# Performance work log

Hardware: AMD Instinct MI355X
Metric: run time of the kernel (lower is better)

Reference implementation:

```python
import jax, jax.numpy as jnp
import numpy as np

KERNEL_SIZE = 5
GROUP_SIZE = 1
SCALE = 2


def setup_inputs() -> dict:
    key = jax.random.key(0)
    k1, k2 = jax.random.split(key)
    N, C, H, W = 2, 256, 128, 128
    features = jax.random.normal(k1, (N, C, H, W), dtype=jnp.float32)
    masks = jax.random.uniform(
        k2, (N, KERNEL_SIZE * KERNEL_SIZE * GROUP_SIZE, H * SCALE, W * SCALE),
        dtype=jnp.float32)
    return {"features": features, "masks": masks}


def reference(features, masks):
    # CARAFE: content-aware reassembly upsampling.
    # out[n,c,i,j] = sum_{dy,dx} feat[n,c, i//s + dy - r, j//s + dx - r]
    #                * masks[n, g*K*K + dy*K + dx, i, j]
    K, G, s = KERNEL_SIZE, GROUP_SIZE, SCALE
    N, C, H, W = features.shape
    Cg = C // G
    K2 = K * K
    r = K // 2
    # zero-pad spatially and gather all K*K shifted views -> (N, C, K2, H, W)
    fp = jnp.pad(features, ((0, 0), (0, 0), (r, r), (r, r)))
    patches = jnp.stack(
        [fp[:, :, dy:dy + H, dx:dx + W] for dy in range(K) for dx in range(K)],
        axis=2)
    patches = patches.reshape(N, G, Cg, K2, H, W)
    # masks at output resolution; split each output pixel into (src_pixel, subpixel)
    m = masks.reshape(N, G, K2, H, s, W, s)
    # weighted reduce over the kernel window, broadcast over channels in group
    out = jnp.einsum('ngckhw,ngkhawb->ngchawb', patches, m)
    return out.reshape(N, C, H * s, W * s)
```

## Files before the change

### kernel.cpp

```cpp
#include <hip/hip_runtime.h>

#define KK 5
#define RR 2
#define N_ 2
#define C_ 256
#define H_ 128
#define W_ 128
#define H2 256
#define W2 256
#define TH 16
#define TW 16
#define CCHUNK 8
#define PH 20
#define PW 20
#define PHPW 400
#define HW (H_*W_)
#define HW2 (H2*W2)
#define DEPTH 4

__global__ __launch_bounds__(256) void carafe_kernel(
    const float* __restrict__ feat,
    const float* __restrict__ masks,
    float* __restrict__ out)
{
    __shared__ float patch[2 * PHPW * 4];

    const int tid = threadIdx.x;
    const int tx = tid & 15;
    const int ty = tid >> 4;

    const int chunk = blockIdx.x & 31;
    const int tile  = blockIdx.x >> 5;
    const int bx = tile & 7;
    const int by = tile >> 3;
    const int c0 = chunk * CCHUNK;
    const int n  = blockIdx.y;

    const int i0 = by * TH + ty;
    const int j0 = bx * TW + tx;
    const int gy0 = by * TH - RR;
    const int gx0 = bx * TW - RR;

    const float* fbase = feat + (size_t)(n * C_ + c0) * HW;
    #pragma unroll
    for (int r = 0; r < 4; ++r) {
        const int idx = tid + r * 256;
        if (idx < 2 * PHPW) {
            const int G  = idx / PHPW;
            const int p  = idx - G * PHPW;
            const int py = p / PW;
            const int px = p - py * PW;
            const int gy = gy0 + py;
            const int gx = gx0 + px;
            float4 v = make_float4(0.f, 0.f, 0.f, 0.f);
            if ((unsigned)gy < (unsigned)H_ && (unsigned)gx < (unsigned)W_) {
                const float* fp = fbase + (4 * G) * HW + gy * W_ + gx;
                v.x = fp[0];
                v.y = fp[HW];
                v.z = fp[2 * HW];
                v.w = fp[3 * HW];
            }
            *reinterpret_cast<float4*>(&patch[G * 1600 + p * 4]) = v;
        }
    }

    const float* mb = masks + ((size_t)n * (KK * KK) * H2 + (size_t)(2 * i0)) * W2 + 2 * j0;
    float2 q0[DEPTH], q1[DEPTH];
    #pragma unroll
    for (int t = 0; t < DEPTH; ++t) {
        q0[t] = *reinterpret_cast<const float2*>(mb + (size_t)t * HW2);
        q1[t] = *reinterpret_cast<const float2*>(mb + (size_t)t * HW2 + W2);
    }
    __syncthreads();

    float acc[CCHUNK][2][2] = {};
    const int p0 = ty * PW + tx;

    #pragma unroll
    for (int k = 0; k < KK * KK; ++k) {
        const float2 m0 = q0[k % DEPTH];
        const float2 m1 = q1[k % DEPTH];
        if (k + DEPTH < KK * KK) {
            q0[k % DEPTH] = *reinterpret_cast<const float2*>(mb + (size_t)(k + DEPTH) * HW2);
            q1[k % DEPTH] = *reinterpret_cast<const float2*>(mb + (size_t)(k + DEPTH) * HW2 + W2);
        }
        const int dy = k / KK;
        const int dx = k - KK * dy;
        const int P  = p0 + dy * PW + dx;
        const float4 v0 = *reinterpret_cast<const float4*>(&patch[P * 4]);
        const float4 v1 = *reinterpret_cast<const float4*>(&patch[1600 + P * 4]);

        acc[0][0][0] += v0.x * m0.x;  acc[0][0][1] += v0.x * m0.y;
        acc[0][1][0] += v0.x * m1.x;  acc[0][1][1] += v0.x * m1.y;
        acc[1][0][0] += v0.y * m0.x;  acc[1][0][1] += v0.y * m0.y;
        acc[1][1][0] += v0.y * m1.x;  acc[1][1][1] += v0.y * m1.y;
        acc[2][0][0] += v0.z * m0.x;  acc[2][0][1] += v0.z * m0.y;
        acc[2][1][0] += v0.z * m1.x;  acc[2][1][1] += v0.z * m1.y;
        acc[3][0][0] += v0.w * m0.x;  acc[3][0][1] += v0.w * m0.y;
        acc[3][1][0] += v0.w * m1.x;  acc[3][1][1] += v0.w * m1.y;
        acc[4][0][0] += v1.x * m0.x;  acc[4][0][1] += v1.x * m0.y;
        acc[4][1][0] += v1.x * m1.x;  acc[4][1][1] += v1.x * m1.y;
        acc[5][0][0] += v1.y * m0.x;  acc[5][0][1] += v1.y * m0.y;
        acc[5][1][0] += v1.y * m1.x;  acc[5][1][1] += v1.y * m1.y;
        acc[6][0][0] += v1.z * m0.x;  acc[6][0][1] += v1.z * m0.y;
        acc[6][1][0] += v1.z * m1.x;  acc[6][1][1] += v1.z * m1.y;
        acc[7][0][0] += v1.w * m0.x;  acc[7][0][1] += v1.w * m0.y;
        acc[7][1][0] += v1.w * m1.x;  acc[7][1][1] += v1.w * m1.y;
    }

    float* ob = out + ((size_t)(n * C_ + c0) * H2 + (size_t)(2 * i0)) * W2 + 2 * j0;
    #pragma unroll
    for (int c = 0; c < CCHUNK; ++c) {
        *reinterpret_cast<float2*>(ob)      = make_float2(acc[c][0][0], acc[c][0][1]);
        *reinterpret_cast<float2*>(ob + W2) = make_float2(acc[c][1][0], acc[c][1][1]);
        ob += (size_t)HW2;
    }
}

extern "C" void kernel_launch(void* const* d_in, const int* in_sizes, int n_in,
                              void* d_out, int out_size, void* d_ws, size_t ws_size,
                              hipStream_t stream) {
    const float* feat  = (const float*)d_in[0];
    const float* masks = (const float*)d_in[1];
    float* out = (float*)d_out;

    dim3 grid(32 * 64,
              N_);
    carafe_kernel<<<grid, dim3(256), 0, stream>>>(feat, masks, out);
}
```

Before: 52.14 us.

## Split channel chunk across two thread halves with 512-thread blocks

```diff
diff --git a/kernel.cpp b/kernel.cpp
--- a/kernel.cpp
+++ b/kernel.cpp
@@ -17,8 +17,9 @@
 #define HW (H_*W_)
 #define HW2 (H2*W2)
 #define DEPTH 4
+#define BLK 512
 
-__global__ __launch_bounds__(256) void carafe_kernel(
+__global__ __launch_bounds__(BLK) void carafe_kernel(
     const float* __restrict__ feat,
     const float* __restrict__ masks,
     float* __restrict__ out)
@@ -26,8 +27,10 @@
     __shared__ float patch[2 * PHPW * 4];
 
     const int tid = threadIdx.x;
-    const int tx = tid & 15;
-    const int ty = tid >> 4;
+    const int q   = tid >> 8;
+    const int pp  = tid & 255;
+    const int tx  = pp & 15;
+    const int ty  = pp >> 4;
 
     const int chunk = blockIdx.x & 31;
     const int tile  = blockIdx.x >> 5;
@@ -43,8 +46,8 @@
 
     const float* fbase = feat + (size_t)(n * C_ + c0) * HW;
     #pragma unroll
-    for (int r = 0; r < 4; ++r) {
-        const int idx = tid + r * 256;
+    for (int r = 0; r < 2; ++r) {
+        const int idx = tid + r * BLK;
         if (idx < 2 * PHPW) {
             const int G  = idx / PHPW;
             const int p  = idx - G * PHPW;
@@ -73,8 +76,9 @@
     }
     __syncthreads();
 
-    float acc[CCHUNK][2][2] = {};
+    float acc[4][2][2] = {};
     const int p0 = ty * PW + tx;
+    const int plane = q * 1600;
 
     #pragma unroll
     for (int k = 0; k < KK * KK; ++k) {
@@ -87,32 +91,23 @@
         const int dy = k / KK;
         const int dx = k - KK * dy;
         const int P  = p0 + dy * PW + dx;
-        const float4 v0 = *reinterpret_cast<const float4*>(&patch[P * 4]);
-        const float4 v1 = *reinterpret_cast<const float4*>(&patch[1600 + P * 4]);
+        const float4 v = *reinterpret_cast<const float4*>(&patch[plane + P * 4]);
 
-        acc[0][0][0] += v0.x * m0.x;  acc[0][0][1] += v0.x * m0.y;
-        acc[0][1][0] += v0.x * m1.x;  acc[0][1][1] += v0.x * m1.y;
-        acc[1][0][0] += v0.y * m0.x;  acc[1][0][1] += v0.y * m0.y;
-        acc[1][1][0] += v0.y * m1.x;  acc[1][1][1] += v0.y * m1.y;
-        acc[2][0][0] += v0.z * m0.x;  acc[2][0][1] += v0.z * m0.y;
-        acc[2][1][0] += v0.z * m1.x;  acc[2][1][1] += v0.z * m1.y;
-        acc[3][0][0] += v0.w * m0.x;  acc[3][0][1] += v0.w * m0.y;
-        acc[3][1][0] += v0.w * m1.x;  acc[3][1][1] += v0.w * m1.y;
-        acc[4][0][0] += v1.x * m0.x;  acc[4][0][1] += v1.x * m0.y;
-        acc[4][1][0] += v1.x * m1.x;  acc[4][1][1] += v1.x * m1.y;
-        acc[5][0][0] += v1.y * m0.x;  acc[5][0][1] += v1.y * m0.y;
-        acc[5][1][0] += v1.y * m1.x;  acc[5][1][1] += v1.y * m1.y;
-        acc[6][0][0] += v1.z * m0.x;  acc[6][0][1] += v1.z * m0.y;
-        acc[6][1][0] += v1.z * m1.x;  acc[6][1][1] += v1.z * m1.y;
-        acc[7][0][0] += v1.w * m0.x;  acc[7][0][1] += v1.w * m0.y;
-        acc[7][1][0] += v1.w * m1.x;  acc[7][1][1] += v1.w * m1.y;
+        acc[0][0][0] += v.x * m0.x;  acc[0][0][1] += v.x * m0.y;
+        acc[0][1][0] += v.x * m1.x;  acc[0][1][1] += v.x * m1.y;
+        acc[1][0][0] += v.y * m0.x;  acc[1][0][1] += v.y * m0.y;
+        acc[1][1][0] += v.y * m1.x;  acc[1][1][1] += v.y * m1.y;
+        acc[2][0][0] += v.z * m0.x;  acc[2][0][1] += v.z * m0.y;
+        acc[2][1][0] += v.z * m1.x;  acc[2][1][1] += v.z * m1.y;
+        acc[3][0][0] += v.w * m0.x;  acc[3][0][1] += v.w * m0.y;
+        acc[3][1][0] += v.w * m1.x;  acc[3][1][1] += v.w * m1.y;
     }
 
-    float* ob = out + ((size_t)(n * C_ + c0) * H2 + (size_t)(2 * i0)) * W2 + 2 * j0;
+    float* ob = out + ((size_t)(n * C_ + c0 + 4 * q) * H2 + (size_t)(2 * i0)) * W2 + 2 * j0;
     #pragma unroll
-    for (int c = 0; c < CCHUNK; ++c) {
-        *reinterpret_cast<float2*>(ob)      = make_float2(acc[c][0][0], acc[c][0][1]);
-        *reinterpret_cast<float2*>(ob + W2) = make_float2(acc[c][1][0], acc[c][1][1]);
+    for (int t = 0; t < 4; ++t) {
+        *reinterpret_cast<float2*>(ob)      = make_float2(acc[t][0][0], acc[t][0][1]);
+        *reinterpret_cast<float2*>(ob + W2) = make_float2(acc[t][1][0], acc[t][1][1]);
         ob += (size_t)HW2;
     }
 }
@@ -126,5 +121,5 @@
 
     dim3 grid(32 * 64,
               N_);
-    carafe_kernel<<<grid, dim3(256), 0, stream>>>(feat, masks, out);
+    carafe_kernel<<<grid, dim3(BLK), 0, stream>>>(feat, masks, out);
 }
```

After: 68.93 us. 1.32x slower.

## Use 32x8 tiles and remap block IDs so each XCD shares mask tiles

Applied to the files above, without the earlier changes.

```diff
diff --git a/kernel.cpp b/kernel.cpp
--- a/kernel.cpp
+++ b/kernel.cpp
@@ -8,12 +8,13 @@
 #define W_ 128
 #define H2 256
 #define W2 256
-#define TH 16
-#define TW 16
+#define TW 32
+#define TH 8
 #define CCHUNK 8
-#define PH 20
-#define PW 20
-#define PHPW 400
+#define PHh 12
+#define PWw 36
+#define NPIX (PHh*PWw)
+#define PLANE (NPIX*4)
 #define HW (H_*W_)
 #define HW2 (H2*W2)
 #define DEPTH 4
@@ -23,18 +24,22 @@
     const float* __restrict__ masks,
     float* __restrict__ out)
 {
-    __shared__ float patch[2 * PHPW * 4];
+    __shared__ float patch[2 * PLANE];
 
     const int tid = threadIdx.x;
-    const int tx = tid & 15;
-    const int ty = tid >> 4;
+    const int tx = tid & 31;
+    const int ty = tid >> 5;
 
-    const int chunk = blockIdx.x & 31;
-    const int tile  = blockIdx.x >> 5;
-    const int bx = tile & 7;
-    const int by = tile >> 3;
-    const int c0 = chunk * CCHUNK;
-    const int n  = blockIdx.y;
+    const int bid   = blockIdx.x;
+    const int xcd   = bid & 7;
+    const int s     = bid >> 3;
+    const int chunk = s & 31;
+    const int tn    = xcd * 16 + (s >> 5);
+    const int tile  = tn & 63;
+    const int n     = tn >> 6;
+    const int bx    = tile & 3;
+    const int by    = tile >> 2;
+    const int c0    = chunk * CCHUNK;
 
     const int i0 = by * TH + ty;
     const int j0 = bx * TW + tx;
@@ -45,11 +50,11 @@
     #pragma unroll
     for (int r = 0; r < 4; ++r) {
         const int idx = tid + r * 256;
-        if (idx < 2 * PHPW) {
-            const int G  = idx / PHPW;
-            const int p  = idx - G * PHPW;
-            const int py = p / PW;
-            const int px = p - py * PW;
+        if (idx < 2 * NPIX) {
+            const int G  = idx >= NPIX;
+            const int p  = idx - G * NPIX;
+            const int py = p / PWw;
+            const int px = p - py * PWw;
             const int gy = gy0 + py;
             const int gx = gx0 + px;
             float4 v = make_float4(0.f, 0.f, 0.f, 0.f);
@@ -60,7 +65,7 @@
                 v.z = fp[2 * HW];
                 v.w = fp[3 * HW];
             }
-            *reinterpret_cast<float4*>(&patch[G * 1600 + p * 4]) = v;
+            *reinterpret_cast<float4*>(&patch[G * PLANE + p * 4]) = v;
         }
     }
 
@@ -74,7 +79,7 @@
     __syncthreads();
 
     float acc[CCHUNK][2][2] = {};
-    const int p0 = ty * PW + tx;
+    const int p0 = ty * PWw + tx;
 
     #pragma unroll
     for (int k = 0; k < KK * KK; ++k) {
@@ -86,9 +91,9 @@
         }
         const int dy = k / KK;
         const int dx = k - KK * dy;
-        const int P  = p0 + dy * PW + dx;
+        const int P  = p0 + dy * PWw + dx;
         const float4 v0 = *reinterpret_cast<const float4*>(&patch[P * 4]);
-        const float4 v1 = *reinterpret_cast<const float4*>(&patch[1600 + P * 4]);
+        const float4 v1 = *reinterpret_cast<const float4*>(&patch[PLANE + P * 4]);
 
         acc[0][0][0] += v0.x * m0.x;  acc[0][0][1] += v0.x * m0.y;
         acc[0][1][0] += v0.x * m1.x;  acc[0][1][1] += v0.x * m1.y;
@@ -124,7 +129,5 @@
     const float* masks = (const float*)d_in[1];
     float* out = (float*)d_out;
 
-    dim3 grid(32 * 64,
-              N_);
-    carafe_kernel<<<grid, dim3(256), 0, stream>>>(feat, masks, out);
+    carafe_kernel<<<dim3(4096), dim3(256), 0, stream>>>(feat, masks, out);
 }
```

After: 49.00 us. 6.0% less time.
